# Performance work log

Hardware: AMD Instinct MI355X
Metric: run time of the kernel (lower is better)

## Reference

```python
import jax, jax.numpy as jnp
import numpy as np

NUM_BITS = 8
VMIN, VMAX = 0.0, 1.0
THRESH = 4.0
K_SYN = 32


def gray_code_encode(x):
    # (batch, features) -> (batch, features*NUM_BITS) binary float bits
    norm = (jnp.clip(x, VMIN, VMAX) - VMIN) / (VMAX - VMIN)
    levels = jnp.round(norm * (2 ** NUM_BITS - 1)).astype(jnp.int32)
    gray = levels ^ (levels >> 1)
    bit_pos = jnp.arange(NUM_BITS, dtype=jnp.int32)
    bits = ((gray[..., None] >> bit_pos) & 1).astype(jnp.float32)
    return bits.reshape(x.shape[0], -1)


def _make_sparse_weight(key, n_neurons, prev_size):
    # k random synapses per neuron with +/-1 weights (rest zero), as in
    # _initialise_layer_weights (standard, non-dynamic path)
    kc, ks = jax.random.split(key)
    cols = jax.random.randint(kc, (n_neurons, K_SYN), 0, prev_size)
    signs = jax.random.randint(ks, (n_neurons, K_SYN), 0, 2).astype(jnp.float32) * 2 - 1
    rows = jnp.broadcast_to(jnp.arange(n_neurons)[:, None], (n_neurons, K_SYN))
    return jnp.zeros((n_neurons, prev_size), jnp.float32).at[rows, cols].set(signs)


def setup_inputs() -> dict:
    key = jax.random.key(0)
    kx, k0, k1, k2, ko = jax.random.split(key, 5)
    batch, feat = 512, 256
    hidden, classes, n_hidden_layers = 4096, 1000, 3
    enc = feat * NUM_BITS  # 2048
    x = jax.random.uniform(kx, (batch, feat), dtype=jnp.float32)
    W0 = _make_sparse_weight(k0, hidden, enc)
    W1 = _make_sparse_weight(k1, hidden, hidden)
    W2 = _make_sparse_weight(k2, hidden, hidden)
    out_w = jax.random.normal(ko, (n_hidden_layers, hidden, classes), dtype=jnp.float32) * 0.01
    return {"x": x, "W0": W0, "W1": W1, "W2": W2, "out_w": out_w}


def reference(x, W0, W1, W2, out_w):
    prev = gray_code_encode(x)  # (b, enc)
    out = jnp.zeros((x.shape[0], out_w.shape[-1]), jnp.float32)
    for i, W in enumerate((W0, W1, W2)):
        z = prev @ W.T                                  # (b, hidden)
        prev = (z >= THRESH).astype(jnp.float32)        # binary activation
        out = out + prev @ out_w[i]                     # accumulate per-layer
    return out
```

## Files before the change

### kernel.cpp

```cpp
#include <hip/hip_runtime.h>
#include <stdint.h>

typedef unsigned long long u64;
typedef __attribute__((ext_vector_type(8))) short bf16x8;
typedef __attribute__((ext_vector_type(4))) float f32x4;
typedef __attribute__((ext_vector_type(4))) unsigned u32x4;

#define BATCH 512
#define FEAT 256
#define ENC 2048
#define HID 4096
#define CLS 1000
#define KTOT 12288
#define NSPLIT 16
#define KSPLIT 768
#define PARTLD 1024

#define OFF_ENC2   0
#define OFF_ACT2   131072
#define OFF_TABLE  917504
#define OFF_SGN    1703936
#define OFF_WT     2097152
#define OFF_PART   27262976
#define PART_BYTES (16ull * 512 * 1024 * 4)
#define WS_NEED    (OFF_PART + PART_BYTES)

static __device__ inline unsigned short f2bf(float f) {
    unsigned u = __float_as_uint(f);
    return (unsigned short)((u + 0x7FFFu + ((u >> 16) & 1u)) >> 16);
}

static __device__ inline void gld16(const void* g, void* s) {
    __builtin_amdgcn_global_load_lds((const __attribute__((address_space(1))) void*)g,
                                     (__attribute__((address_space(3))) void*)s, 16, 0, 0);
}

__global__ void __launch_bounds__(256)
k_prep(const float* __restrict__ x, u64* __restrict__ enc2,
       const float* __restrict__ W0, const float* __restrict__ W1,
       const float* __restrict__ W2,
       uint16_t* __restrict__ table, unsigned* __restrict__ bits,
       const float* __restrict__ out_w, short* __restrict__ wt) {
    __shared__ short tile[64 * 68];
    __shared__ int cnt4[4];
    __shared__ int lneg[4];
    int bid = blockIdx.x;
    int t = threadIdx.x;
    int lane = t & 63;
    int wv = t >> 6;

    if (bid < 512) {
        int wid = bid * 4 + wv;
        int f = wid >> 3, bg = wid & 7;
        float v = x[(size_t)(bg * 64 + lane) * FEAT + f];
        v = fminf(fmaxf(v, 0.0f), 1.0f);
        int lev = (int)rintf(v * 255.0f);
        unsigned gray = (unsigned)(lev ^ (lev >> 1));
        u64 w = 0;
        #pragma unroll
        for (int bit = 0; bit < 8; ++bit) {
            u64 m = __ballot((gray >> bit) & 1u);
            if (lane == bit) w = m;
        }
        if (lane < 8) enc2[(size_t)bg * ENC + f * 8 + lane] = w;
        return;
    }
    if (bid < 5632) {
        int wsid = (bid - 512) * 4 + wv;
        int row, base, cidx;
        if (wsid < HID) { row = wsid; base = 0; cidx = wv; }
        else {
            int w2 = wsid - HID;
            row = HID + (w2 >> 1);
            base = (w2 & 1) * 2048;
            cidx = wv >> 1;
        }
        uint16_t* te = table + (size_t)row * 32;
        if (lane < 8) ((u64*)te)[lane] = 0;
        if (t < 4) { cnt4[t] = 0; lneg[t] = 0; }
        __syncthreads();
        const float* Wr;
        if (row < HID)          Wr = W0 + (size_t)row * ENC;
        else if (row < 2 * HID) Wr = W1 + (size_t)(row - HID) * HID + base;
        else                    Wr = W2 + (size_t)(row - 2 * HID) * HID + base;
        const u32x4* p4 = (const u32x4*)Wr;
        u32x4 v[8];
        #pragma unroll
        for (int j = 0; j < 8; ++j) v[j] = __builtin_nontemporal_load(p4 + j * 64 + lane);
        #pragma unroll
        for (int j = 0; j < 8; ++j) {
            unsigned a0 = v[j].x, a1 = v[j].y, a2 = v[j].z, a3 = v[j].w;
            if (a0 | a1 | a2 | a3) {
                int col0 = base + j * 256 + lane * 4;
                if (a0) { int s = atomicAdd(&cnt4[cidx], 1); te[s] = (uint16_t)col0;
                          if (a0 >> 31) atomicOr(&lneg[cidx], (int)(1u << s)); }
                if (a1) { int s = atomicAdd(&cnt4[cidx], 1); te[s] = (uint16_t)(col0 + 1);
                          if (a1 >> 31) atomicOr(&lneg[cidx], (int)(1u << s)); }
                if (a2) { int s = atomicAdd(&cnt4[cidx], 1); te[s] = (uint16_t)(col0 + 2);
                          if (a2 >> 31) atomicOr(&lneg[cidx], (int)(1u << s)); }
                if (a3) { int s = atomicAdd(&cnt4[cidx], 1); te[s] = (uint16_t)(col0 + 3);
                          if (a3 >> 31) atomicOr(&lneg[cidx], (int)(1u << s)); }
            }
        }
        __syncthreads();
        if (lane == 0) {
            int cnt = cnt4[cidx];
            unsigned nb = (unsigned)lneg[cidx];
            unsigned vb = (cnt >= 32) ? 0xFFFFFFFFu : ((1u << cnt) - 1u);
            uint2 pr; pr.x = nb; pr.y = vb;
            *(uint2*)(bits + (size_t)row * 2) = pr;
        }
        return;
    }
    {
        int b2 = bid - 5632;
        int kt = b2 % 192, ct = b2 / 192;
        int k0 = kt * 64, c0 = ct * 64;
        {
            int rrow = t >> 4, c4 = t & 15;
            int c = c0 + c4 * 4;
            #pragma unroll
            for (int rd = 0; rd < 4; ++rd) {
                int kl = rd * 16 + rrow;
                f32x4 vv;
                if (c < CLS)
                    vv = __builtin_nontemporal_load(
                        (const f32x4*)&out_w[(size_t)(k0 + kl) * CLS + c]);
                else { vv.x = 0.0f; vv.y = 0.0f; vv.z = 0.0f; vv.w = 0.0f; }
                short* d = &tile[kl * 68 + c4 * 4];
                d[0] = (short)f2bf(vv.x); d[1] = (short)f2bf(vv.y);
                d[2] = (short)f2bf(vv.z); d[3] = (short)f2bf(vv.w);
            }
        }
        __syncthreads();
        {
            int chunk = t & 7, cl2 = t >> 3;
            #pragma unroll
            for (int rd = 0; rd < 2; ++rd) {
                int c_local = rd * 32 + cl2;
                int c = c0 + c_local;
                unsigned s8[8];
                #pragma unroll
                for (int j = 0; j < 8; ++j)
                    s8[j] = (unsigned)(unsigned short)tile[(chunk * 8 + j) * 68 + c_local];
                uint4 pk;
                pk.x = s8[0] | (s8[1] << 16);
                pk.y = s8[2] | (s8[3] << 16);
                pk.z = s8[4] | (s8[5] << 16);
                pk.w = s8[6] | (s8[7] << 16);
                *(uint4*)&wt[(size_t)c * KTOT + k0 + ((chunk ^ (c & 7)) * 8)] = pk;
            }
        }
    }
}

__global__ void __launch_bounds__(64)
k_layer(const u64* __restrict__ prev2, int Kwords,
        const uint16_t* __restrict__ table_l, const unsigned* __restrict__ bits_l,
        u64* __restrict__ actout) {
    int g = blockIdx.x >> 3, bg = blockIdx.x & 7;
    int lane = threadIdx.x;
    int n = (g << 6) + lane;
    const u64* prow = prev2 + (size_t)bg * Kwords;
    const uint4* tq = (const uint4*)(table_l + (size_t)n * 32);
    uint4 cw0 = tq[0], cw1 = tq[1], cw2 = tq[2], cw3 = tq[3];
    uint2 bv = *(const uint2*)(bits_l + (size_t)n * 2);
    unsigned negb = bv.x, valb = bv.y;

    u64 P[4][4];
    uint4 cwa[4] = {cw0, cw1, cw2, cw3};
    #pragma unroll
    for (int k = 0; k < 4; ++k) {
        unsigned w0 = cwa[k].x, w1 = cwa[k].y, w2 = cwa[k].z, w3 = cwa[k].w;
        unsigned cc[8] = { w0 & 0xFFFFu, w0 >> 16, w1 & 0xFFFFu, w1 >> 16,
                           w2 & 0xFFFFu, w2 >> 16, w3 & 0xFFFFu, w3 >> 16 };
        u64 u[8];
        #pragma unroll
        for (int e = 0; e < 8; ++e) {
            int j = (k << 3) + e;
            u64 w = prow[cc[e]];
            u64 negm = 0ull - (u64)((negb >> j) & 1u);
            u64 vm   = 0ull - (u64)((valb >> j) & 1u);
            u[e] = (w ^ negm) & vm;
        }
        u64 s0, c0, s1, c1, s2, c2, b0, c3, t2, d0, b1, d1;
        { u64 t = u[0] ^ u[1]; s0 = t ^ u[2]; c0 = (u[0] & u[1]) | (u[2] & t); }
        { u64 t = u[3] ^ u[4]; s1 = t ^ u[5]; c1 = (u[3] & u[4]) | (u[5] & t); }
        s2 = u[6] ^ u[7]; c2 = u[6] & u[7];
        { u64 t = s0 ^ s1; b0 = t ^ s2; c3 = (s0 & s1) | (s2 & t); }
        { u64 t = c0 ^ c1; t2 = t ^ c2; d0 = (c0 & c1) | (c2 & t); }
        b1 = t2 ^ c3; d1 = t2 & c3;
        P[k][0] = b0; P[k][1] = b1; P[k][2] = d0 ^ d1; P[k][3] = d0 & d1;
    }
    u64 A[5], B[5], U[6];
    { u64 c;
      { u64 t = P[0][0] ^ P[1][0]; A[0] = t; c = P[0][0] & P[1][0]; }
      #pragma unroll
      for (int i = 1; i < 4; ++i) {
          u64 t = P[0][i] ^ P[1][i]; A[i] = t ^ c; c = (P[0][i] & P[1][i]) | (c & t); }
      A[4] = c; }
    { u64 c;
      { u64 t = P[2][0] ^ P[3][0]; B[0] = t; c = P[2][0] & P[3][0]; }
      #pragma unroll
      for (int i = 1; i < 4; ++i) {
          u64 t = P[2][i] ^ P[3][i]; B[i] = t ^ c; c = (P[2][i] & P[3][i]) | (c & t); }
      B[4] = c; }
    { u64 c;
      { u64 t = A[0] ^ B[0]; U[0] = t; c = A[0] & B[0]; }
      #pragma unroll
      for (int i = 1; i < 5; ++i) {
          u64 t = A[i] ^ B[i]; U[i] = t ^ c; c = (A[i] & B[i]) | (c & t); }
      U[5] = c; }
    int K = 60 - __popc(negb & valb);
    u64 c = 0;
    #pragma unroll
    for (int i = 0; i < 6; ++i) {
        u64 ki = 0ull - (u64)((K >> i) & 1);
        u64 t = U[i] ^ ki;
        c = (U[i] & ki) | (c & t);
    }
    actout[(size_t)bg * HID + n] = c;
}

template<int MODE>
__global__ void __launch_bounds__(256)
k_gemm(const u64* __restrict__ act2, const short* __restrict__ wt,
       float* __restrict__ out, float* __restrict__ part) {
    __shared__ __attribute__((aligned(16))) short As[128 * 64];
    __shared__ __attribute__((aligned(16))) short Bs[128 * 64];
    int bid = blockIdx.x;
    int mt = bid & 3, nt = (bid >> 2) & 7, ks = bid >> 5;
    int tid = threadIdx.x, lane = tid & 63;
    int wv = tid >> 6, waveM = wv & 1, waveN = wv >> 1;
    int quad = lane >> 4, cl = lane & 15;
    f32x4 acc[4][4] = {};
    const char* Bb = (const char*)(wt + (size_t)nt * 128 * KTOT + ks * KSPLIT);
    int r = tid >> 3, sub = tid & 7;
    for (int kk = 0; kk < KSPLIT; kk += 64) {
        #pragma unroll
        for (int rd = 0; rd < 4; ++rd) {
            size_t go = (size_t)(r + rd * 32) * (KTOT * 2) + kk * 2 + sub * 16;
            gld16(Bb + go, &Bs[(tid + rd * 256) * 8]);
        }
        {
            int kabs = ks * KSPLIT + kk;
            int l = kabs >> 12, nk = kabs & 4095;
            #pragma unroll
            for (int i = 0; i < 4; ++i) {
                int item = i * 256 + tid;
                int rr = item >> 3, gg = item & 7;
                const u64* w8 = act2 + ((size_t)(l * 8 + mt * 2 + (rr >> 6))) * HID + nk + gg * 8;
                int bl = rr & 63;
                unsigned sh[8];
                #pragma unroll
                for (int j = 0; j < 8; ++j)
                    sh[j] = (unsigned)((w8[j] >> bl) & 1ull) * 0x3F80u;
                uint4 pk;
                pk.x = sh[0] | (sh[1] << 16);
                pk.y = sh[2] | (sh[3] << 16);
                pk.z = sh[4] | (sh[5] << 16);
                pk.w = sh[6] | (sh[7] << 16);
                *(uint4*)&As[rr * 64 + ((gg ^ (rr & 7)) * 8)] = pk;
            }
        }
        __syncthreads();
        #pragma unroll
        for (int s = 0; s < 2; ++s) {
            int xr = ((s * 4 + quad) ^ (cl & 7)) * 8;
            bf16x8 af[4], bfr[4];
            #pragma unroll
            for (int mf = 0; mf < 4; ++mf)
                af[mf] = *(const bf16x8*)&As[(waveM * 64 + mf * 16 + cl) * 64 + xr];
            #pragma unroll
            for (int nf = 0; nf < 4; ++nf)
                bfr[nf] = *(const bf16x8*)&Bs[(waveN * 64 + nf * 16 + cl) * 64 + xr];
            #pragma unroll
            for (int mf = 0; mf < 4; ++mf)
                #pragma unroll
                for (int nf = 0; nf < 4; ++nf)
                    acc[mf][nf] = __builtin_amdgcn_mfma_f32_16x16x32_bf16(
                        af[mf], bfr[nf], acc[mf][nf], 0, 0, 0);
        }
        __syncthreads();
    }
    if (MODE == 0) {
        float* pbase = part + (size_t)ks * (BATCH * PARTLD);
        #pragma unroll
        for (int mf = 0; mf < 4; ++mf)
            #pragma unroll
            for (int nf = 0; nf < 4; ++nf) {
                int cp = nt * 128 + waveN * 64 + nf * 16 + cl;
                #pragma unroll
                for (int rr = 0; rr < 4; ++rr) {
                    int mg = mt * 128 + waveM * 64 + mf * 16 + quad * 4 + rr;
                    pbase[(size_t)mg * PARTLD + cp] = acc[mf][nf][rr];
                }
            }
    } else {
        #pragma unroll
        for (int mf = 0; mf < 4; ++mf)
            #pragma unroll
            for (int nf = 0; nf < 4; ++nf) {
                int cp = nt * 128 + waveN * 64 + nf * 16 + cl;
                if (cp < CLS) {
                    #pragma unroll
                    for (int rr = 0; rr < 4; ++rr) {
                        int mg = mt * 128 + waveM * 64 + mf * 16 + quad * 4 + rr;
                        atomicAdd(&out[(size_t)mg * CLS + cp], acc[mf][nf][rr]);
                    }
                }
            }
    }
}

__global__ void k_reduce(const float* __restrict__ part, float* __restrict__ out) {
    int idx = blockIdx.x * blockDim.x + threadIdx.x;
    if (idx >= BATCH * (CLS / 4)) return;
    int b = idx / (CLS / 4), c4 = idx - b * (CLS / 4);
    f32x4 s = {0.f, 0.f, 0.f, 0.f};
    #pragma unroll
    for (int sp = 0; sp < NSPLIT; ++sp) {
        f32x4 v = *(const f32x4*)&part[((size_t)sp * BATCH + b) * PARTLD + c4 * 4];
        s.x += v.x; s.y += v.y; s.z += v.z; s.w += v.w;
    }
    *(f32x4*)&out[(size_t)b * CLS + c4 * 4] = s;
}

extern "C" void kernel_launch(void* const* d_in, const int* in_sizes, int n_in,
                              void* d_out, int out_size, void* d_ws, size_t ws_size,
                              hipStream_t stream) {
    const float* x     = (const float*)d_in[0];
    const float* W0    = (const float*)d_in[1];
    const float* W1    = (const float*)d_in[2];
    const float* W2    = (const float*)d_in[3];
    const float* out_w = (const float*)d_in[4];
    float* out = (float*)d_out;
    char* ws = (char*)d_ws;

    u64*      enc2   = (u64*)(ws + OFF_ENC2);
    u64*      act2   = (u64*)(ws + OFF_ACT2);
    uint16_t* table  = (uint16_t*)(ws + OFF_TABLE);
    unsigned* bits   = (unsigned*)(ws + OFF_SGN);
    short*    wt     = (short*)(ws + OFF_WT);
    float*    part   = (float*)(ws + OFF_PART);

    int use_part = (ws_size >= (size_t)WS_NEED) ? 1 : 0;

    hipLaunchKernelGGL(k_prep, dim3(8704), dim3(256), 0, stream,
                       x, enc2, W0, W1, W2, table, bits, out_w, wt);
    if (!use_part)
        (void)hipMemsetAsync(d_out, 0, (size_t)BATCH * CLS * sizeof(float), stream);

    hipLaunchKernelGGL(k_layer, dim3(512), dim3(64), 0, stream,
                       enc2, ENC, table, bits, act2);
    hipLaunchKernelGGL(k_layer, dim3(512), dim3(64), 0, stream,
                       act2, HID, table + (size_t)HID * 32, bits + (size_t)HID * 2,
                       act2 + 8 * HID);
    hipLaunchKernelGGL(k_layer, dim3(512), dim3(64), 0, stream,
                       act2 + 8 * HID, HID, table + (size_t)2 * HID * 32,
                       bits + (size_t)2 * HID * 2, act2 + 16 * HID);
    if (use_part) {
        hipLaunchKernelGGL((k_gemm<0>), dim3(512), dim3(256), 0, stream,
                           act2, wt, out, part);
        hipLaunchKernelGGL(k_reduce, dim3((BATCH * (CLS / 4) + 255) / 256), dim3(256), 0,
                           stream, part, out);
    } else {
        hipLaunchKernelGGL((k_gemm<1>), dim3(512), dim3(256), 0, stream,
                           act2, wt, out, part);
    }
}
```

Baseline: 241.9 us.

## Fuse encode and three sparse layers into one kernel, fold reduce into GEMM

Moves the gray-code encoding out of the prep kernel and fuses it with all three sparse binary layers into a single kernel with one 1024-thread block per batch group. Activations stay in LDS between layers, replacing three small launches and their global round trips. The split-K partial reduction now runs inside the GEMM: the last-arriving block per tile, found through an atomic counter, does the sum, so the separate reduce kernel goes away. In exchange the fused layer kernel runs on only 8 blocks, which leaves most of the GPU idle during the sequential layer phase.

```diff
diff --git a/kernel.cpp b/kernel.cpp
--- a/kernel.cpp
+++ b/kernel.cpp
@@ -16,7 +16,7 @@
 #define KSPLIT 768
 #define PARTLD 1024
 
-#define OFF_ENC2   0
+#define OFF_CNT    0
 #define OFF_ACT2   131072
 #define OFF_TABLE  917504
 #define OFF_SGN    1703936
@@ -36,8 +36,7 @@
 }
 
 __global__ void __launch_bounds__(256)
-k_prep(const float* __restrict__ x, u64* __restrict__ enc2,
-       const float* __restrict__ W0, const float* __restrict__ W1,
+k_prep(const float* __restrict__ W0, const float* __restrict__ W1,
        const float* __restrict__ W2,
        uint16_t* __restrict__ table, unsigned* __restrict__ bits,
        const float* __restrict__ out_w, short* __restrict__ wt) {
@@ -49,24 +48,8 @@
     int lane = t & 63;
     int wv = t >> 6;
 
-    if (bid < 512) {
-        int wid = bid * 4 + wv;
-        int f = wid >> 3, bg = wid & 7;
-        float v = x[(size_t)(bg * 64 + lane) * FEAT + f];
-        v = fminf(fmaxf(v, 0.0f), 1.0f);
-        int lev = (int)rintf(v * 255.0f);
-        unsigned gray = (unsigned)(lev ^ (lev >> 1));
-        u64 w = 0;
-        #pragma unroll
-        for (int bit = 0; bit < 8; ++bit) {
-            u64 m = __ballot((gray >> bit) & 1u);
-            if (lane == bit) w = m;
-        }
-        if (lane < 8) enc2[(size_t)bg * ENC + f * 8 + lane] = w;
-        return;
-    }
-    if (bid < 5632) {
-        int wsid = (bid - 512) * 4 + wv;
+    if (bid < 5120) {
+        int wsid = bid * 4 + wv;
         int row, base, cidx;
         if (wsid < HID) { row = wsid; base = 0; cidx = wv; }
         else {
@@ -113,7 +96,7 @@
         return;
     }
     {
-        int b2 = bid - 5632;
+        int b2 = bid - 5120;
         int kt = b2 % 192, ct = b2 / 192;
         int k0 = kt * 64, c0 = ct * 64;
         {
@@ -154,21 +137,15 @@
     }
 }
 
-__global__ void __launch_bounds__(64)
-k_layer(const u64* __restrict__ prev2, int Kwords,
-        const uint16_t* __restrict__ table_l, const unsigned* __restrict__ bits_l,
-        u64* __restrict__ actout) {
-    int g = blockIdx.x >> 3, bg = blockIdx.x & 7;
-    int lane = threadIdx.x;
-    int n = (g << 6) + lane;
-    const u64* prow = prev2 + (size_t)bg * Kwords;
+static __device__ __forceinline__ u64 unit_csa(
+    const u64* __restrict__ prow,
+    const uint16_t* __restrict__ table_l, const unsigned* __restrict__ bits_l, int n) {
     const uint4* tq = (const uint4*)(table_l + (size_t)n * 32);
-    uint4 cw0 = tq[0], cw1 = tq[1], cw2 = tq[2], cw3 = tq[3];
+    uint4 cwa[4] = {tq[0], tq[1], tq[2], tq[3]};
     uint2 bv = *(const uint2*)(bits_l + (size_t)n * 2);
     unsigned negb = bv.x, valb = bv.y;
 
     u64 P[4][4];
-    uint4 cwa[4] = {cw0, cw1, cw2, cw3};
     #pragma unroll
     for (int k = 0; k < 4; ++k) {
         unsigned w0 = cwa[k].x, w1 = cwa[k].y, w2 = cwa[k].z, w3 = cwa[k].w;
@@ -219,13 +196,181 @@
         u64 t = U[i] ^ ki;
         c = (U[i] & ki) | (c & t);
     }
-    actout[(size_t)bg * HID + n] = c;
-}
-
-template<int MODE>
+    return c;
+}
+
+__global__ void __launch_bounds__(1024)
+k_net2(const float* __restrict__ x,
+       const uint16_t* __restrict__ table, const unsigned* __restrict__ bits,
+       u64* __restrict__ act2, int* __restrict__ cnt) {
+    __shared__ u64 bufA[4096];
+    __shared__ u64 bufB[4096];
+    int bg = blockIdx.x;
+    int tid = threadIdx.x, w = tid >> 6, lane = tid & 63;
+
+    if (bg == 0 && tid < 64) cnt[tid] = 0;
+
+    {
+        const f32x4* xr = (const f32x4*)(x + (size_t)(bg * 64 + lane) * FEAT + w * 16);
+        f32x4 xv[4] = {xr[0], xr[1], xr[2], xr[3]};
+        #pragma unroll
+        for (int ff = 0; ff < 16; ++ff) {
+            float v = xv[ff >> 2][ff & 3];
+            v = fminf(fmaxf(v, 0.0f), 1.0f);
+            int lev = (int)rintf(v * 255.0f);
+            unsigned gray = (unsigned)(lev ^ (lev >> 1));
+            u64 keep = 0;
+            #pragma unroll
+            for (int bit = 0; bit < 8; ++bit) {
+                u64 m = __ballot((gray >> bit) & 1u);
+                if (lane == bit) keep = m;
+            }
+            if (lane < 8) bufA[(w * 16 + ff) * 8 + lane] = keep;
+        }
+    }
+    __syncthreads();
+
+    {
+        u64* outG = act2 + (size_t)bg * HID;
+        #pragma unroll
+        for (int i = 0; i < 4; ++i) {
+            int n = (w + i * 16) * 64 + lane;
+            u64 c = unit_csa(bufA, table, bits, n);
+            bufB[n] = c; outG[n] = c;
+        }
+    }
+    __syncthreads();
+    {
+        u64* outG = act2 + (size_t)(8 + bg) * HID;
+        const uint16_t* tl = table + (size_t)HID * 32;
+        const unsigned* bl = bits + (size_t)HID * 2;
+        #pragma unroll
+        for (int i = 0; i < 4; ++i) {
+            int n = (w + i * 16) * 64 + lane;
+            u64 c = unit_csa(bufB, tl, bl, n);
+            bufA[n] = c; outG[n] = c;
+        }
+    }
+    __syncthreads();
+    {
+        u64* outG = act2 + (size_t)(16 + bg) * HID;
+        const uint16_t* tl = table + (size_t)2 * HID * 32;
+        const unsigned* bl = bits + (size_t)2 * HID * 2;
+        #pragma unroll
+        for (int i = 0; i < 4; ++i) {
+            int n = (w + i * 16) * 64 + lane;
+            u64 c = unit_csa(bufA, tl, bl, n);
+            outG[n] = c;
+        }
+    }
+}
+
+static __device__ __forceinline__ void gemm_core(
+    const u64* __restrict__ act2, const short* __restrict__ wt,
+    float* __restrict__ part, short* As, short* Bs,
+    int mt, int nt, int ks, int tid) {
+    int lane = tid & 63;
+    int wv = tid >> 6, waveM = wv & 1, waveN = wv >> 1;
+    int quad = lane >> 4, cl = lane & 15;
+    f32x4 acc[4][4] = {};
+    const char* Bb = (const char*)(wt + (size_t)nt * 128 * KTOT + ks * KSPLIT);
+    int r = tid >> 3, sub = tid & 7;
+    for (int kk = 0; kk < KSPLIT; kk += 64) {
+        #pragma unroll
+        for (int rd = 0; rd < 4; ++rd) {
+            size_t go = (size_t)(r + rd * 32) * (KTOT * 2) + kk * 2 + sub * 16;
+            gld16(Bb + go, &Bs[(tid + rd * 256) * 8]);
+        }
+        {
+            int kabs = ks * KSPLIT + kk;
+            int l = kabs >> 12, nk = kabs & 4095;
+            #pragma unroll
+            for (int i = 0; i < 4; ++i) {
+                int item = i * 256 + tid;
+                int rr = item >> 3, gg = item & 7;
+                const u64* w8 = act2 + ((size_t)(l * 8 + mt * 2 + (rr >> 6))) * HID + nk + gg * 8;
+                int bl = rr & 63;
+                unsigned sh[8];
+                #pragma unroll
+                for (int j = 0; j < 8; ++j)
+                    sh[j] = (unsigned)((w8[j] >> bl) & 1ull) * 0x3F80u;
+                uint4 pk;
+                pk.x = sh[0] | (sh[1] << 16);
+                pk.y = sh[2] | (sh[3] << 16);
+                pk.z = sh[4] | (sh[5] << 16);
+                pk.w = sh[6] | (sh[7] << 16);
+                *(uint4*)&As[rr * 64 + ((gg ^ (rr & 7)) * 8)] = pk;
+            }
+        }
+        __syncthreads();
+        #pragma unroll
+        for (int s = 0; s < 2; ++s) {
+            int xr = ((s * 4 + quad) ^ (cl & 7)) * 8;
+            bf16x8 af[4], bfr[4];
+            #pragma unroll
+            for (int mf = 0; mf < 4; ++mf)
+                af[mf] = *(const bf16x8*)&As[(waveM * 64 + mf * 16 + cl) * 64 + xr];
+            #pragma unroll
+            for (int nf = 0; nf < 4; ++nf)
+                bfr[nf] = *(const bf16x8*)&Bs[(waveN * 64 + nf * 16 + cl) * 64 + xr];
+            #pragma unroll
+            for (int mf = 0; mf < 4; ++mf)
+                #pragma unroll
+                for (int nf = 0; nf < 4; ++nf)
+                    acc[mf][nf] = __builtin_amdgcn_mfma_f32_16x16x32_bf16(
+                        af[mf], bfr[nf], acc[mf][nf], 0, 0, 0);
+        }
+        __syncthreads();
+    }
+    float* pbase = part + (size_t)ks * (BATCH * PARTLD);
+    #pragma unroll
+    for (int mf = 0; mf < 4; ++mf)
+        #pragma unroll
+        for (int nf = 0; nf < 4; ++nf) {
+            int cp = nt * 128 + waveN * 64 + nf * 16 + cl;
+            #pragma unroll
+            for (int rr = 0; rr < 4; ++rr) {
+                int mg = mt * 128 + waveM * 64 + mf * 16 + quad * 4 + rr;
+                pbase[(size_t)mg * PARTLD + cp] = acc[mf][nf][rr];
+            }
+        }
+}
+
 __global__ void __launch_bounds__(256)
-k_gemm(const u64* __restrict__ act2, const short* __restrict__ wt,
-       float* __restrict__ out, float* __restrict__ part) {
+k_gemm3(const u64* __restrict__ act2, const short* __restrict__ wt,
+        float* __restrict__ out, float* __restrict__ part, int* __restrict__ cnt) {
+    __shared__ __attribute__((aligned(16))) short As[128 * 64];
+    __shared__ __attribute__((aligned(16))) short Bs[128 * 64];
+    __shared__ int amlast;
+    int bid = blockIdx.x;
+    int nt = bid & 7, ks = (bid >> 3) & 15, mt = bid >> 7;
+    int tid = threadIdx.x;
+    gemm_core(act2, wt, part, As, Bs, mt, nt, ks, tid);
+    __threadfence();
+    if (tid == 0) amlast = (atomicAdd(&cnt[mt * 8 + nt], 1) == NSPLIT - 1) ? 1 : 0;
+    __syncthreads();
+    if (!amlast) return;
+    int r = tid >> 1, ch = (tid & 1) * 64;
+    int mg = mt * 128 + r;
+    const float* pb = part + (size_t)mg * PARTLD + nt * 128 + ch;
+    #pragma unroll
+    for (int c4 = 0; c4 < 16; ++c4) {
+        int cp = nt * 128 + ch + c4 * 4;
+        if (cp < CLS) {
+            f32x4 s = {0.f, 0.f, 0.f, 0.f};
+            #pragma unroll
+            for (int sp = 0; sp < NSPLIT; ++sp) {
+                f32x4 v = *(const f32x4*)&pb[(size_t)sp * (BATCH * PARTLD) + c4 * 4];
+                s.x += v.x; s.y += v.y; s.z += v.z; s.w += v.w;
+            }
+            *(f32x4*)&out[(size_t)mg * CLS + cp] = s;
+        }
+    }
+}
+
+__global__ void __launch_bounds__(256)
+k_gemm_atomic(const u64* __restrict__ act2, const short* __restrict__ wt,
+              float* __restrict__ out) {
     __shared__ __attribute__((aligned(16))) short As[128 * 64];
     __shared__ __attribute__((aligned(16))) short Bs[128 * 64];
     int bid = blockIdx.x;
@@ -283,47 +428,19 @@
         }
         __syncthreads();
     }
-    if (MODE == 0) {
-        float* pbase = part + (size_t)ks * (BATCH * PARTLD);
-        #pragma unroll
-        for (int mf = 0; mf < 4; ++mf)
-            #pragma unroll
-            for (int nf = 0; nf < 4; ++nf) {
-                int cp = nt * 128 + waveN * 64 + nf * 16 + cl;
+    #pragma unroll
+    for (int mf = 0; mf < 4; ++mf)
+        #pragma unroll
+        for (int nf = 0; nf < 4; ++nf) {
+            int cp = nt * 128 + waveN * 64 + nf * 16 + cl;
+            if (cp < CLS) {
                 #pragma unroll
                 for (int rr = 0; rr < 4; ++rr) {
                     int mg = mt * 128 + waveM * 64 + mf * 16 + quad * 4 + rr;
-                    pbase[(size_t)mg * PARTLD + cp] = acc[mf][nf][rr];
+                    atomicAdd(&out[(size_t)mg * CLS + cp], acc[mf][nf][rr]);
                 }
             }
-    } else {
-        #pragma unroll
-        for (int mf = 0; mf < 4; ++mf)
-            #pragma unroll
-            for (int nf = 0; nf < 4; ++nf) {
-                int cp = nt * 128 + waveN * 64 + nf * 16 + cl;
-                if (cp < CLS) {
-                    #pragma unroll
-                    for (int rr = 0; rr < 4; ++rr) {
-                        int mg = mt * 128 + waveM * 64 + mf * 16 + quad * 4 + rr;
-                        atomicAdd(&out[(size_t)mg * CLS + cp], acc[mf][nf][rr]);
-                    }
-                }
-            }
-    }
-}
-
-__global__ void k_reduce(const float* __restrict__ part, float* __restrict__ out) {
-    int idx = blockIdx.x * blockDim.x + threadIdx.x;
-    if (idx >= BATCH * (CLS / 4)) return;
-    int b = idx / (CLS / 4), c4 = idx - b * (CLS / 4);
-    f32x4 s = {0.f, 0.f, 0.f, 0.f};
-    #pragma unroll
-    for (int sp = 0; sp < NSPLIT; ++sp) {
-        f32x4 v = *(const f32x4*)&part[((size_t)sp * BATCH + b) * PARTLD + c4 * 4];
-        s.x += v.x; s.y += v.y; s.z += v.z; s.w += v.w;
-    }
-    *(f32x4*)&out[(size_t)b * CLS + c4 * 4] = s;
+        }
 }
 
 extern "C" void kernel_launch(void* const* d_in, const int* in_sizes, int n_in,
@@ -337,35 +454,25 @@
     float* out = (float*)d_out;
     char* ws = (char*)d_ws;
 
-    u64*      enc2   = (u64*)(ws + OFF_ENC2);
-    u64*      act2   = (u64*)(ws + OFF_ACT2);
-    uint16_t* table  = (uint16_t*)(ws + OFF_TABLE);
-    unsigned* bits   = (unsigned*)(ws + OFF_SGN);
-    short*    wt     = (short*)(ws + OFF_WT);
-    float*    part   = (float*)(ws + OFF_PART);
+    int*            cnt    = (int*)(ws + OFF_CNT);
+    u64*            act2   = (u64*)(ws + OFF_ACT2);
+    uint16_t*       table  = (uint16_t*)(ws + OFF_TABLE);
+    unsigned*       bits   = (unsigned*)(ws + OFF_SGN);
+    short*          wt     = (short*)(ws + OFF_WT);
+    float*          part   = (float*)(ws + OFF_PART);
 
     int use_part = (ws_size >= (size_t)WS_NEED) ? 1 : 0;
 
-    hipLaunchKernelGGL(k_prep, dim3(8704), dim3(256), 0, stream,
-                       x, enc2, W0, W1, W2, table, bits, out_w, wt);
-    if (!use_part)
+    hipLaunchKernelGGL(k_prep, dim3(8192), dim3(256), 0, stream,
+                       W0, W1, W2, table, bits, out_w, wt);
+    hipLaunchKernelGGL(k_net2, dim3(8), dim3(1024), 0, stream,
+                       x, table, bits, act2, cnt);
+    if (use_part) {
+        hipLaunchKernelGGL(k_gemm3, dim3(512), dim3(256), 0, stream,
+                           act2, wt, out, part, cnt);
+    } else {
         (void)hipMemsetAsync(d_out, 0, (size_t)BATCH * CLS * sizeof(float), stream);
-
-    hipLaunchKernelGGL(k_layer, dim3(512), dim3(64), 0, stream,
-                       enc2, ENC, table, bits, act2);
-    hipLaunchKernelGGL(k_layer, dim3(512), dim3(64), 0, stream,
-                       act2, HID, table + (size_t)HID * 32, bits + (size_t)HID * 2,
-                       act2 + 8 * HID);
-    hipLaunchKernelGGL(k_layer, dim3(512), dim3(64), 0, stream,
-                       act2 + 8 * HID, HID, table + (size_t)2 * HID * 32,
-                       bits + (size_t)2 * HID * 2, act2 + 16 * HID);
-    if (use_part) {
-        hipLaunchKernelGGL((k_gemm<0>), dim3(512), dim3(256), 0, stream,
-                           act2, wt, out, part);
-        hipLaunchKernelGGL(k_reduce, dim3((BATCH * (CLS / 4) + 255) / 256), dim3(256), 0,
-                           stream, part, out);
-    } else {
-        hipLaunchKernelGGL((k_gemm<1>), dim3(512), dim3(256), 0, stream,
-                           act2, wt, out, part);
-    }
-}
+        hipLaunchKernelGGL(k_gemm_atomic, dim3(512), dim3(256), 0, stream,
+                           act2, wt, out);
+    }
+}
```

After: 423.4 us. 75.0% more time.
